# Optimization experiments

Measured on AMD Instinct MI355X. Metric: run time of the kernel, lower is better.

Reference implementation:

```python
import jax, jax.numpy as jnp
import numpy as np

D_MODEL = 1024
NUM_HEADS = 16
HEAD_DIM = D_MODEL // NUM_HEADS


def setup_inputs() -> dict:
    key = jax.random.key(0)
    ks = jax.random.split(key, 8)
    B, S = 4, 1024
    scale = 1.0 / np.sqrt(D_MODEL)
    return {
        "x": jax.random.normal(ks[0], (B, S, D_MODEL), jnp.float32),
        "tokens": jax.random.normal(ks[1], (B, 1, D_MODEL), jnp.float32),
        "Wq": jax.random.normal(ks[2], (D_MODEL, D_MODEL), jnp.float32) * scale,
        "bq": jnp.zeros((D_MODEL,), jnp.float32),
        "Wk": jax.random.normal(ks[3], (D_MODEL, D_MODEL), jnp.float32) * scale,
        "bk": jnp.zeros((D_MODEL,), jnp.float32),
        "Wv": jax.random.normal(ks[4], (D_MODEL, D_MODEL), jnp.float32) * scale,
        "bv": jnp.zeros((D_MODEL,), jnp.float32),
    }


def _split_heads(t):
    # [B, S, D] -> [B, H, S, hd]
    B, S, _ = t.shape
    return t.reshape(B, S, NUM_HEADS, HEAD_DIM).transpose(0, 2, 1, 3)


def reference(x, tokens, Wq, bq, Wk, bk, Wv, bv):
    # Projections (torch Linear: y = x @ W.T + b)
    Q = _split_heads(x @ Wq.T + bq)          # [B,H,S,hd]
    K = _split_heads(x @ Wk.T + bk)
    V = _split_heads(x @ Wv.T + bv)
    tQ = _split_heads(tokens @ Wq.T + bq)    # [B,H,1,hd] -> broadcast
    tK = _split_heads(tokens @ Wk.T + bk)
    cQ = Q + tQ
    cK = K + tK
    scores = jnp.einsum("bhqd,bhkd->bhqk", cQ, cK) / jnp.sqrt(jnp.float32(HEAD_DIM))
    attn = jax.nn.softmax(scores, axis=-1)
    out = jnp.einsum("bhqk,bhkd->bhqd", attn, V)  # [B,H,S,hd]
    B, H, S, hd = out.shape
    return out.transpose(0, 2, 1, 3).reshape(B, S, D_MODEL)
```

## Files before the change

### kernel.cpp

```cpp
#include <hip/hip_runtime.h>
#include <hip/hip_bf16.h>


typedef __bf16 bf16;
typedef __bf16 bf16x8 __attribute__((ext_vector_type(8)));
typedef float  f32x4  __attribute__((ext_vector_type(4)));

#define LOG2E 1.4426950408889634f

__device__ __forceinline__ void gll16(const void* g, void* l) {
  __builtin_amdgcn_global_load_lds(
      (const __attribute__((address_space(1))) unsigned int*)g,
      (__attribute__((address_space(3))) unsigned int*)l, 16, 0, 0);
}

__device__ __forceinline__ unsigned cvtpk(float a, float b) {
  unsigned r;
  asm("v_cvt_pk_bf16_f32 %0, %1, %2" : "=v"(r) : "v"(a), "v"(b));
  return r;
}

__global__ void prep_kernel(const float* __restrict__ x, const float* __restrict__ tok,
                            const float* __restrict__ wq, const float* __restrict__ wk,
                            const float* __restrict__ wv,
                            bf16* __restrict__ xb, bf16* __restrict__ xt,
                            bf16* __restrict__ wdst) {
  const int bid = blockIdx.x;
  if (bid < 2048) {
    const size_t e = ((size_t)bid * 256 + threadIdx.x) * 8;
    const int b = (int)(e >> 20);
    const int d = (int)(e & 1023);
    const float4 a0 = *(const float4*)(x + e);
    const float4 a1 = *(const float4*)(x + e + 4);
    const float4 t0 = *(const float4*)(tok + b * 1024 + d);
    const float4 t1 = *(const float4*)(tok + b * 1024 + d + 4);
    bf16x8 vb, vt;
    vb[0]=(bf16)a0.x; vb[1]=(bf16)a0.y; vb[2]=(bf16)a0.z; vb[3]=(bf16)a0.w;
    vb[4]=(bf16)a1.x; vb[5]=(bf16)a1.y; vb[6]=(bf16)a1.z; vb[7]=(bf16)a1.w;
    vt[0]=(bf16)(a0.x+t0.x); vt[1]=(bf16)(a0.y+t0.y); vt[2]=(bf16)(a0.z+t0.z); vt[3]=(bf16)(a0.w+t0.w);
    vt[4]=(bf16)(a1.x+t1.x); vt[5]=(bf16)(a1.y+t1.y); vt[6]=(bf16)(a1.z+t1.z); vt[7]=(bf16)(a1.w+t1.w);
    *(bf16x8*)(xb + e) = vb;
    *(bf16x8*)(xt + e) = vt;
  } else {
    const size_t e = ((size_t)(bid - 2048) * 256 + threadIdx.x) * 8;
    const float* src; size_t off;
    if (e < (size_t)(1u<<20))      { src = wq; off = e; }
    else if (e < (size_t)(2u<<20)) { src = wk; off = e - (1u<<20); }
    else                           { src = wv; off = e - (2u<<20); }
    const float4 a0 = *(const float4*)(src + off);
    const float4 a1 = *(const float4*)(src + off + 4);
    bf16x8 v;
    v[0]=(bf16)a0.x; v[1]=(bf16)a0.y; v[2]=(bf16)a0.z; v[3]=(bf16)a0.w;
    v[4]=(bf16)a1.x; v[5]=(bf16)a1.y; v[6]=(bf16)a1.z; v[7]=(bf16)a1.w;
    *(bf16x8*)(wdst + e) = v;
  }
}

__global__ __launch_bounds__(256, 3) void qkv_gemm_kernel(
    const bf16* __restrict__ xt, const bf16* __restrict__ xb,
    const bf16* __restrict__ wq, const bf16* __restrict__ wk, const bf16* __restrict__ wv,
    const float* __restrict__ bq, const float* __restrict__ bk, const float* __restrict__ bv,
    bf16* __restrict__ cq, bf16* __restrict__ ck, bf16* __restrict__ vt)
{
  __shared__ __align__(16) char LDSG[49152];
  char* As = LDSG;
  char* Bs = LDSG + 24576;
  const int t = threadIdx.x, w = t >> 6, l = t & 63, g = l >> 4, c = l & 15;
  const int wr = w >> 1, wc = w & 1;
  const int wgid = blockIdx.x;
  const int xcd = wgid & 7;
  const int p = wgid >> 3;
  const int z = p >> 5;
  const int q = p & 31;
  const bf16 *A, *B; const float* bias; bf16* outp;
  int tm, tn;
  if (z < 2) { tm = xcd * 4 + (q & 3); tn = q >> 2; }
  else       { tm = q >> 2; tn = xcd * 4 + (q & 3); }
  if (z == 0)      { A = xt; B = wq; bias = bq; outp = cq; }
  else if (z == 1) { A = xt; B = wk; bias = bk; outp = ck; }
  else             { A = wv; B = xb; bias = bv; outp = vt; }
  const int m0 = tm * 128, n0 = tn * 128;

  f32x4 acc[4][4] = {};

  const int u = (t & 7) ^ ((t >> 3) & 7);
  const size_t ssw = (size_t)(2 * (t >> 3) + (u >> 2)) * 2048 + (size_t)(u & 3) * 16;
  const char* aga = (const char*)A + (size_t)m0 * 2048 + ssw;
  const char* bga = (const char*)B + (size_t)n0 * 2048 + ssw;

#define GSTAGE(slot, kt)                                                 \
  {                                                                      \
    const size_t ko = (size_t)(kt) * 64;            \
    char* ad = As + (slot) * 8192 + t * 16;                              \
    char* bd = Bs + (slot) * 8192 + t * 16;                              \
    gll16(aga + ko,          ad);                                        \
    gll16(aga + ko + 131072, ad + 4096);               \
    gll16(bga + ko,          bd);                                        \
    gll16(bga + ko + 131072, bd + 4096);                                 \
  }

  GSTAGE(0, 0);
  GSTAGE(1, 1);
  int st = 2;
  int s  = 0;
  for (int kt = 0; kt < 32; ++kt) {
    if (kt < 31) { asm volatile("s_waitcnt vmcnt(4)" ::: "memory"); }
    else         { asm volatile("s_waitcnt vmcnt(0)" ::: "memory"); }
    __builtin_amdgcn_sched_barrier(0);
    __builtin_amdgcn_s_barrier();
    if (kt < 30) GSTAGE(st, kt + 2);

    const char* Ab = As + s * 8192;
    const char* Bb = Bs + s * 8192;
    bf16x8 af[4], bfr[4];
#pragma unroll
    for (int mf = 0; mf < 4; ++mf) {
      const int mrow = wr * 64 + mf * 16 + c;
      af[mf] = *(const bf16x8*)(Ab + (mrow >> 1) * 128 +
                                (((((mrow & 1) << 2) + g) ^ ((mrow >> 1) & 7)) << 4));
    }
#pragma unroll
    for (int nf = 0; nf < 4; ++nf) {
      const int nrow = wc * 64 + nf * 16 + c;
      bfr[nf] = *(const bf16x8*)(Bb + (nrow >> 1) * 128 +
                                 (((((nrow & 1) << 2) + g) ^ ((nrow >> 1) & 7)) << 4));
    }
    __builtin_amdgcn_s_setprio(1);
#pragma unroll
    for (int mf = 0; mf < 4; ++mf)
#pragma unroll
      for (int nf = 0; nf < 4; ++nf)
        acc[mf][nf] = __builtin_amdgcn_mfma_f32_16x16x32_bf16(af[mf], bfr[nf], acc[mf][nf], 0, 0, 0);
    __builtin_amdgcn_s_setprio(0);
    s  = (s  == 2) ? 0 : s + 1;
    st = (st == 2) ? 0 : st + 1;
  }
#undef GSTAGE

  if (z < 2) {
    const float sc = (z == 0) ? 0.125f * LOG2E : 1.0f;
#pragma unroll
    for (int mf = 0; mf < 4; ++mf)
#pragma unroll
      for (int nf = 0; nf < 4; ++nf) {
        const int n = n0 + wc * 64 + nf * 16 + c;
        const int h = n >> 6, d = n & 63;
        const float bsum = 2.0f * bias[n];
#pragma unroll
        for (int r = 0; r < 4; ++r) {
          const int m = m0 + wr * 64 + mf * 16 + g * 4 + r;
          const int b = m >> 10, s2 = m & 1023;
          outp[(((size_t)(b * 16 + h)) * 1024 + s2) * 64 + d] = (bf16)((acc[mf][nf][r] + bsum) * sc);
        }
      }
  } else {
#pragma unroll
    for (int mf = 0; mf < 4; ++mf)
#pragma unroll
      for (int nf = 0; nf < 4; ++nf) {
        const int n = n0 + wc * 64 + nf * 16 + c;
        const int b = n >> 10, s2 = n & 1023;
#pragma unroll
        for (int r = 0; r < 4; ++r) {
          const int m = m0 + wr * 64 + mf * 16 + g * 4 + r;
          const int h = m >> 6, d = m & 63;
          outp[(((size_t)(b * 16 + h)) * 64 + d) * 1024 + s2] = (bf16)(acc[mf][nf][r] + bias[m]);
        }
      }
  }
}

__global__ __launch_bounds__(512) void attn_kernel(
    const bf16* __restrict__ cq, const bf16* __restrict__ ck, const bf16* __restrict__ vt,
    float* __restrict__ out)
{
  __shared__ __align__(16) char LDS[49152];
  const int t = threadIdx.x, w = t >> 6, l = t & 63, g = l >> 4, c = l & 15;
  const int wgid = blockIdx.x;
  const int xcd = wgid & 7;
  const int p_ = wgid >> 3;
  const int bh = xcd * 8 + (p_ >> 3);
  const int qt = p_ & 7;
  const int b = bh >> 4, h = bh & 15;
  const bf16* cqb = cq + (size_t)bh * 65536;
  const bf16* ckb = ck + (size_t)bh * 65536;
  const bf16* vtb = vt + (size_t)bh * 65536;
  const int q0 = qt * 128 + w * 16;

  bf16x8 qf[2];
#pragma unroll
  for (int kf = 0; kf < 2; ++kf)
    qf[kf] = *(const bf16x8*)(cqb + (size_t)(q0 + c) * 64 + kf * 32 + g * 8);

  f32x4 o[4] = {};
  float m = -INFINITY, lsum = 0.f;

  const int r_ = t >> 3;
  const int sch = (t & 7) ^ (r_ & 7);
  const int kap = ((r_ >> 4) & 1) * 32 + ((r_ >> 2) & 3) * 8 + ((r_ >> 5) & 1) * 4 + (r_ & 3);
  const size_t ksrc = (size_t)kap * 128 + (size_t)sch * 16;
  const size_t vsrc = (size_t)r_ * 2048 + (size_t)sch * 16;

#define STAGE(slot, idx)                                                 \
  {                                                                      \
    const char* kgb = (const char*)ckb + (size_t)(idx) * 8192;           \
    const char* vgb = (const char*)vtb + (size_t)(idx) * 128;            \
    gll16(kgb + ksrc, LDS + (slot) * 8192 + t * 16);                     \
    gll16(vgb + vsrc, LDS + 24576 + (slot) * 8192 + t * 16);             \
  }

  STAGE(0, 0);
  STAGE(1, 1);
  int st = 2;
  int s  = 0;
  for (int idx = 0; idx < 16; ++idx) {
    if (idx < 15) { asm volatile("s_waitcnt vmcnt(2)" ::: "memory"); }
    else          { asm volatile("s_waitcnt vmcnt(0)" ::: "memory"); }
    __builtin_amdgcn_sched_barrier(0);
    __builtin_amdgcn_s_barrier();
    if (idx < 14) STAGE(st, idx + 2);

    const char* Kb = LDS + s * 8192;
    const char* Vb = LDS + 24576 + s * 8192;

    f32x4 sv[4] = {};
    __builtin_amdgcn_s_setprio(1);
#pragma unroll
    for (int kf = 0; kf < 2; ++kf)
#pragma unroll
      for (int nf = 0; nf < 4; ++nf) {
        const int kr = nf * 16 + c;
        bf16x8 kb = *(const bf16x8*)(Kb + kr * 128 + (((kf * 4 + g) ^ (kr & 7)) << 4));
        sv[nf] = __builtin_amdgcn_mfma_f32_16x16x32_bf16(kb, qf[kf], sv[nf], 0, 0, 0);
      }
    __builtin_amdgcn_s_setprio(0);

    const float mx0 = fmaxf(fmaxf(sv[0][0], sv[0][1]), fmaxf(sv[0][2], sv[0][3]));
    const float mx1 = fmaxf(fmaxf(sv[1][0], sv[1][1]), fmaxf(sv[1][2], sv[1][3]));
    const float mx2 = fmaxf(fmaxf(sv[2][0], sv[2][1]), fmaxf(sv[2][2], sv[2][3]));
    const float mx3 = fmaxf(fmaxf(sv[3][0], sv[3][1]), fmaxf(sv[3][2], sv[3][3]));
    float vmax = fmaxf(fmaxf(mx0, mx1), fmaxf(mx2, mx3));
    vmax = fmaxf(vmax, __shfl_xor(vmax, 16, 64));
    vmax = fmaxf(vmax, __shfl_xor(vmax, 32, 64));
    if (!__all(vmax - m <= 8.0f)) {
      const float mnew = fmaxf(m, vmax);
      const float alpha = exp2f(m - mnew);
      m = mnew;
      lsum *= alpha;
#pragma unroll
      for (int nd = 0; nd < 4; ++nd) o[nd] *= alpha;
    }

    float p[4][4];
#pragma unroll
    for (int nf = 0; nf < 4; ++nf)
#pragma unroll
      for (int r = 0; r < 4; ++r)
        p[nf][r] = exp2f(sv[nf][r] - m);
    const float s0_ = (p[0][0] + p[0][1]) + (p[0][2] + p[0][3]);
    const float s1_ = (p[1][0] + p[1][1]) + (p[1][2] + p[1][3]);
    const float s2_ = (p[2][0] + p[2][1]) + (p[2][2] + p[2][3]);
    const float s3_ = (p[3][0] + p[3][1]) + (p[3][2] + p[3][3]);
    float ps = (s0_ + s1_) + (s2_ + s3_);
    ps += __shfl_xor(ps, 16, 64);
    ps += __shfl_xor(ps, 32, 64);
    lsum += ps;

    union { unsigned u[4]; bf16x8 v; } pa0, pa1;
    pa0.u[0] = cvtpk(p[0][0], p[0][1]); pa0.u[1] = cvtpk(p[0][2], p[0][3]);
    pa0.u[2] = cvtpk(p[2][0], p[2][1]); pa0.u[3] = cvtpk(p[2][2], p[2][3]);
    pa1.u[0] = cvtpk(p[1][0], p[1][1]); pa1.u[1] = cvtpk(p[1][2], p[1][3]);
    pa1.u[2] = cvtpk(p[3][0], p[3][1]); pa1.u[3] = cvtpk(p[3][2], p[3][3]);

    __builtin_amdgcn_s_setprio(1);
#pragma unroll
    for (int kf = 0; kf < 2; ++kf) {
      const bf16x8 pav = kf ? pa1.v : pa0.v;
#pragma unroll
      for (int nd = 0; nd < 4; ++nd) {
        const int vr = nd * 16 + c;
        bf16x8 vb = *(const bf16x8*)(Vb + vr * 128 + (((kf * 4 + g) ^ (vr & 7)) << 4));
        o[nd] = __builtin_amdgcn_mfma_f32_16x16x32_bf16(vb, pav, o[nd], 0, 0, 0);
      }
    }
    __builtin_amdgcn_s_setprio(0);

    s  = (s  == 2) ? 0 : s + 1;
    st = (st == 2) ? 0 : st + 1;
  }
#undef STAGE

  __syncthreads();

  const float inv = 1.0f / lsum;
  {
    char* Ob = LDS;
    const int row = w * 16 + c;
#pragma unroll
    for (int nd = 0; nd < 4; ++nd) {
      f32x4 vo = o[nd] * inv;
      const int pch = (nd * 4 + g) ^ (row & 7);
      *(f32x4*)(Ob + row * 256 + (pch << 4)) = vo;
    }
  }
  __syncthreads();
  {
    const int rr = t >> 2;
    float* orow = out + ((size_t)(b * 1024 + qt * 128 + rr)) * 1024 + h * 64;
#pragma unroll
    for (int i = 0; i < 4; ++i) {
      const int ch = (t & 3) + i * 4;
      f32x4 v = *(const f32x4*)(LDS + rr * 256 + ((ch ^ (rr & 7)) << 4));
      *(f32x4*)(orow + ch * 4) = v;
    }
  }
}

extern "C" void kernel_launch(void* const* d_in, const int* in_sizes, int n_in,
                              void* d_out, int out_size, void* d_ws, size_t ws_size,
                              hipStream_t stream) {
  const float* x   = (const float*)d_in[0];
  const float* tok = (const float*)d_in[1];
  const float* Wq  = (const float*)d_in[2];
  const float* bq  = (const float*)d_in[3];
  const float* Wk  = (const float*)d_in[4];
  const float* bk  = (const float*)d_in[5];
  const float* Wv  = (const float*)d_in[6];
  const float* bv  = (const float*)d_in[7];
  float* out = (float*)d_out;
  char* ws = (char*)d_ws;
  bf16* xt  = (bf16*)(ws + (size_t)0);
  bf16* xb  = (bf16*)(ws + ((size_t)8  << 20));
  bf16* wqb = (bf16*)(ws + ((size_t)16 << 20));
  bf16* wkb = (bf16*)(ws + ((size_t)18 << 20));
  bf16* wvb = (bf16*)(ws + ((size_t)20 << 20));
  bf16* cqw = (bf16*)(ws + ((size_t)22 << 20));
  bf16* ckw = (bf16*)(ws + ((size_t)30 << 20));
  bf16* vtw = (bf16*)(ws + ((size_t)38 << 20));

  prep_kernel<<<dim3(3584), dim3(256), 0, stream>>>(x, tok, Wq, Wk, Wv, xb, xt, wqb);
  qkv_gemm_kernel<<<dim3(768), dim3(256), 0, stream>>>(
      xt, xb, wqb, wkb, wvb, bq, bk, bv, cqw, ckw, vtw);
  attn_kernel<<<dim3(512), dim3(512), 0, stream>>>(cqw, ckw, vtw, out);
}
```

Measured before the change: 79.90 us.

## Halve attention workgroup to 4 waves, each processing 32 query rows

```diff
diff --git a/kernel.cpp b/kernel.cpp
--- a/kernel.cpp
+++ b/kernel.cpp
@@ -170,7 +170,7 @@
   }
 }
 
-__global__ __launch_bounds__(512) void attn_kernel(
+__global__ __launch_bounds__(256, 3) void attn_kernel(
     const bf16* __restrict__ cq, const bf16* __restrict__ ck, const bf16* __restrict__ vt,
     float* __restrict__ out)
 {
@@ -185,28 +185,72 @@
   const bf16* cqb = cq + (size_t)bh * 65536;
   const bf16* ckb = ck + (size_t)bh * 65536;
   const bf16* vtb = vt + (size_t)bh * 65536;
-  const int q0 = qt * 128 + w * 16;
-
-  bf16x8 qf[2];
-#pragma unroll
-  for (int kf = 0; kf < 2; ++kf)
-    qf[kf] = *(const bf16x8*)(cqb + (size_t)(q0 + c) * 64 + kf * 32 + g * 8);
-
-  f32x4 o[4] = {};
-  float m = -INFINITY, lsum = 0.f;
+  const int q0 = qt * 128 + w * 32;
+
+  bf16x8 qf0[2], qf1[2];
+#pragma unroll
+  for (int kf = 0; kf < 2; ++kf) {
+    qf0[kf] = *(const bf16x8*)(cqb + (size_t)(q0 + c) * 64 + kf * 32 + g * 8);
+    qf1[kf] = *(const bf16x8*)(cqb + (size_t)(q0 + 16 + c) * 64 + kf * 32 + g * 8);
+  }
+
+  f32x4 o0[4] = {}, o1[4] = {};
+  float m0_ = -INFINITY, ls0 = 0.f;
+  float m1_ = -INFINITY, ls1 = 0.f;
 
   const int r_ = t >> 3;
   const int sch = (t & 7) ^ (r_ & 7);
-  const int kap = ((r_ >> 4) & 1) * 32 + ((r_ >> 2) & 3) * 8 + ((r_ >> 5) & 1) * 4 + (r_ & 3);
-  const size_t ksrc = (size_t)kap * 128 + (size_t)sch * 16;
-  const size_t vsrc = (size_t)r_ * 2048 + (size_t)sch * 16;
+  const int kap = ((r_ >> 4) & 1) * 32 + ((r_ >> 2) & 3) * 8 + (r_ & 3);
+  const size_t ksrc1 = (size_t)kap * 128 + (size_t)sch * 16;
+  const size_t ksrc2 = ksrc1 + 512;
+  const size_t vsrc1 = (size_t)r_ * 2048 + (size_t)sch * 16;
+  const size_t vsrc2 = vsrc1 + 65536;
 
 #define STAGE(slot, idx)                                                 \
   {                                                                      \
     const char* kgb = (const char*)ckb + (size_t)(idx) * 8192;           \
     const char* vgb = (const char*)vtb + (size_t)(idx) * 128;            \
-    gll16(kgb + ksrc, LDS + (slot) * 8192 + t * 16);                     \
-    gll16(vgb + vsrc, LDS + 24576 + (slot) * 8192 + t * 16);             \
+    char* kd = LDS + (slot) * 8192 + t * 16;                             \
+    char* vd = LDS + 24576 + (slot) * 8192 + t * 16;                     \
+    gll16(kgb + ksrc1, kd);                                              \
+    gll16(kgb + ksrc2, kd + 4096);                \
+    gll16(vgb + vsrc1, vd);                                              \
+    gll16(vgb + vsrc2, vd + 4096);                \
+  }
+
+#define SOFTMAX(SV, MM, LS, OO, PA, PB)                                  \
+  {                                                                      \
+    const float mx0 = fmaxf(fmaxf(SV[0][0], SV[0][1]), fmaxf(SV[0][2], SV[0][3])); \
+    const float mx1 = fmaxf(fmaxf(SV[1][0], SV[1][1]), fmaxf(SV[1][2], SV[1][3])); \
+    const float mx2 = fmaxf(fmaxf(SV[2][0], SV[2][1]), fmaxf(SV[2][2], SV[2][3])); \
+    const float mx3 = fmaxf(fmaxf(SV[3][0], SV[3][1]), fmaxf(SV[3][2], SV[3][3])); \
+    float vmax = fmaxf(fmaxf(mx0, mx1), fmaxf(mx2, mx3));                \
+    vmax = fmaxf(vmax, __shfl_xor(vmax, 16, 64));                        \
+    vmax = fmaxf(vmax, __shfl_xor(vmax, 32, 64));                        \
+    if (!__all(vmax - MM <= 8.0f)) {                                     \
+      const float mnew = fmaxf(MM, vmax);                                \
+      const float alpha = exp2f(MM - mnew);                              \
+      MM = mnew; LS *= alpha;                                            \
+      _Pragma("unroll")                                                  \
+      for (int nd = 0; nd < 4; ++nd) OO[nd] *= alpha;                    \
+    }                                                                    \
+    float p[4][4];                                                       \
+    _Pragma("unroll")                                                    \
+    for (int nf = 0; nf < 4; ++nf)                                       \
+      _Pragma("unroll")                                                  \
+      for (int r = 0; r < 4; ++r) p[nf][r] = exp2f(SV[nf][r] - MM);      \
+    const float s0_ = (p[0][0] + p[0][1]) + (p[0][2] + p[0][3]);         \
+    const float s1_ = (p[1][0] + p[1][1]) + (p[1][2] + p[1][3]);         \
+    const float s2_ = (p[2][0] + p[2][1]) + (p[2][2] + p[2][3]);         \
+    const float s3_ = (p[3][0] + p[3][1]) + (p[3][2] + p[3][3]);         \
+    float ps = (s0_ + s1_) + (s2_ + s3_);                                \
+    ps += __shfl_xor(ps, 16, 64);                                        \
+    ps += __shfl_xor(ps, 32, 64);                                        \
+    LS += ps;                                                            \
+    PA.u[0] = cvtpk(p[0][0], p[0][1]); PA.u[1] = cvtpk(p[0][2], p[0][3]); \
+    PA.u[2] = cvtpk(p[2][0], p[2][1]); PA.u[3] = cvtpk(p[2][2], p[2][3]); \
+    PB.u[0] = cvtpk(p[1][0], p[1][1]); PB.u[1] = cvtpk(p[1][2], p[1][3]); \
+    PB.u[2] = cvtpk(p[3][0], p[3][1]); PB.u[3] = cvtpk(p[3][2], p[3][3]); \
   }
 
   STAGE(0, 0);
@@ -214,7 +258,7 @@
   int st = 2;
   int s  = 0;
   for (int idx = 0; idx < 16; ++idx) {
-    if (idx < 15) { asm volatile("s_waitcnt vmcnt(2)" ::: "memory"); }
+    if (idx < 15) { asm volatile("s_waitcnt vmcnt(4)" ::: "memory"); }
     else          { asm volatile("s_waitcnt vmcnt(0)" ::: "memory"); }
     __builtin_amdgcn_sched_barrier(0);
     __builtin_amdgcn_s_barrier();
@@ -223,7 +267,7 @@
     const char* Kb = LDS + s * 8192;
     const char* Vb = LDS + 24576 + s * 8192;
 
-    f32x4 sv[4] = {};
+    f32x4 sv0[4] = {}, sv1[4] = {};
     __builtin_amdgcn_s_setprio(1);
 #pragma unroll
     for (int kf = 0; kf < 2; ++kf)
@@ -231,56 +275,26 @@
       for (int nf = 0; nf < 4; ++nf) {
         const int kr = nf * 16 + c;
         bf16x8 kb = *(const bf16x8*)(Kb + kr * 128 + (((kf * 4 + g) ^ (kr & 7)) << 4));
-        sv[nf] = __builtin_amdgcn_mfma_f32_16x16x32_bf16(kb, qf[kf], sv[nf], 0, 0, 0);
+        sv0[nf] = __builtin_amdgcn_mfma_f32_16x16x32_bf16(kb, qf0[kf], sv0[nf], 0, 0, 0);
+        sv1[nf] = __builtin_amdgcn_mfma_f32_16x16x32_bf16(kb, qf1[kf], sv1[nf], 0, 0, 0);
       }
     __builtin_amdgcn_s_setprio(0);
 
-    const float mx0 = fmaxf(fmaxf(sv[0][0], sv[0][1]), fmaxf(sv[0][2], sv[0][3]));
-    const float mx1 = fmaxf(fmaxf(sv[1][0], sv[1][1]), fmaxf(sv[1][2], sv[1][3]));
-    const float mx2 = fmaxf(fmaxf(sv[2][0], sv[2][1]), fmaxf(sv[2][2], sv[2][3]));
-    const float mx3 = fmaxf(fmaxf(sv[3][0], sv[3][1]), fmaxf(sv[3][2], sv[3][3]));
-    float vmax = fmaxf(fmaxf(mx0, mx1), fmaxf(mx2, mx3));
-    vmax = fmaxf(vmax, __shfl_xor(vmax, 16, 64));
-    vmax = fmaxf(vmax, __shfl_xor(vmax, 32, 64));
-    if (!__all(vmax - m <= 8.0f)) {
-      const float mnew = fmaxf(m, vmax);
-      const float alpha = exp2f(m - mnew);
-      m = mnew;
-      lsum *= alpha;
-#pragma unroll
-      for (int nd = 0; nd < 4; ++nd) o[nd] *= alpha;
-    }
-
-    float p[4][4];
-#pragma unroll
-    for (int nf = 0; nf < 4; ++nf)
-#pragma unroll
-      for (int r = 0; r < 4; ++r)
-        p[nf][r] = exp2f(sv[nf][r] - m);
-    const float s0_ = (p[0][0] + p[0][1]) + (p[0][2] + p[0][3]);
-    const float s1_ = (p[1][0] + p[1][1]) + (p[1][2] + p[1][3]);
-    const float s2_ = (p[2][0] + p[2][1]) + (p[2][2] + p[2][3]);
-    const float s3_ = (p[3][0] + p[3][1]) + (p[3][2] + p[3][3]);
-    float ps = (s0_ + s1_) + (s2_ + s3_);
-    ps += __shfl_xor(ps, 16, 64);
-    ps += __shfl_xor(ps, 32, 64);
-    lsum += ps;
-
-    union { unsigned u[4]; bf16x8 v; } pa0, pa1;
-    pa0.u[0] = cvtpk(p[0][0], p[0][1]); pa0.u[1] = cvtpk(p[0][2], p[0][3]);
-    pa0.u[2] = cvtpk(p[2][0], p[2][1]); pa0.u[3] = cvtpk(p[2][2], p[2][3]);
-    pa1.u[0] = cvtpk(p[1][0], p[1][1]); pa1.u[1] = cvtpk(p[1][2], p[1][3]);
-    pa1.u[2] = cvtpk(p[3][0], p[3][1]); pa1.u[3] = cvtpk(p[3][2], p[3][3]);
+    union { unsigned u[4]; bf16x8 v; } pg0a, pg0b, pg1a, pg1b;
+    SOFTMAX(sv0, m0_, ls0, o0, pg0a, pg0b);
+    SOFTMAX(sv1, m1_, ls1, o1, pg1a, pg1b);
 
     __builtin_amdgcn_s_setprio(1);
 #pragma unroll
     for (int kf = 0; kf < 2; ++kf) {
-      const bf16x8 pav = kf ? pa1.v : pa0.v;
+      const bf16x8 pav0 = kf ? pg0b.v : pg0a.v;
+      const bf16x8 pav1 = kf ? pg1b.v : pg1a.v;
 #pragma unroll
       for (int nd = 0; nd < 4; ++nd) {
         const int vr = nd * 16 + c;
         bf16x8 vb = *(const bf16x8*)(Vb + vr * 128 + (((kf * 4 + g) ^ (vr & 7)) << 4));
-        o[nd] = __builtin_amdgcn_mfma_f32_16x16x32_bf16(vb, pav, o[nd], 0, 0, 0);
+        o0[nd] = __builtin_amdgcn_mfma_f32_16x16x32_bf16(vb, pav0, o0[nd], 0, 0, 0);
+        o1[nd] = __builtin_amdgcn_mfma_f32_16x16x32_bf16(vb, pav1, o1[nd], 0, 0, 0);
       }
     }
     __builtin_amdgcn_s_setprio(0);
@@ -289,27 +303,29 @@
     st = (st == 2) ? 0 : st + 1;
   }
 #undef STAGE
+#undef SOFTMAX
 
   __syncthreads();
 
-  const float inv = 1.0f / lsum;
   {
     char* Ob = LDS;
-    const int row = w * 16 + c;
+    const float inv0 = 1.0f / ls0, inv1 = 1.0f / ls1;
+    const int row0 = w * 32 + c, row1 = w * 32 + 16 + c;
 #pragma unroll
     for (int nd = 0; nd < 4; ++nd) {
-      f32x4 vo = o[nd] * inv;
-      const int pch = (nd * 4 + g) ^ (row & 7);
-      *(f32x4*)(Ob + row * 256 + (pch << 4)) = vo;
+      f32x4 v0 = o0[nd] * inv0;
+      f32x4 v1 = o1[nd] * inv1;
+      *(f32x4*)(Ob + row0 * 256 + (((nd * 4 + g) ^ (row0 & 7)) << 4)) = v0;
+      *(f32x4*)(Ob + row1 * 256 + (((nd * 4 + g) ^ (row1 & 7)) << 4)) = v1;
     }
   }
   __syncthreads();
   {
-    const int rr = t >> 2;
+    const int rr = t >> 1;
     float* orow = out + ((size_t)(b * 1024 + qt * 128 + rr)) * 1024 + h * 64;
 #pragma unroll
-    for (int i = 0; i < 4; ++i) {
-      const int ch = (t & 3) + i * 4;
+    for (int i = 0; i < 8; ++i) {
+      const int ch = i * 2 + (t & 1);
       f32x4 v = *(const f32x4*)(LDS + rr * 256 + ((ch ^ (rr & 7)) << 4));
       *(f32x4*)(orow + ch * 4) = v;
     }
@@ -341,5 +357,5 @@
   prep_kernel<<<dim3(3584), dim3(256), 0, stream>>>(x, tok, Wq, Wk, Wv, xb, xt, wqb);
   qkv_gemm_kernel<<<dim3(768), dim3(256), 0, stream>>>(
       xt, xb, wqb, wkb, wvb, bq, bk, bv, cqw, ckw, vtw);
-  attn_kernel<<<dim3(512), dim3(512), 0, stream>>>(cqw, ckw, vtw, out);
-}
+  attn_kernel<<<dim3(512), dim3(256), 0, stream>>>(cqw, ckw, vtw, out);
+}
```

Result: slower. 83.60 us (+4.6%).
